# Performance work log

Hardware: AMD Instinct MI355X
Metric: run time of the kernel (lower is better)

Reference implementation:

```python
import jax, jax.numpy as jnp
import numpy as np

N = 100000
E = 1600000
IN_CH = 128
HID = 128
OUT_CH = 1
EPS = 1e-5


def setup_inputs() -> dict:
    key = jax.random.key(0)
    ks = jax.random.split(key, 20)
    x = jax.random.normal(ks[0], (N, IN_CH), dtype=jnp.float32)
    edge_index = jax.random.randint(ks[1], (2, E), 0, N, dtype=jnp.int64)

    def lin(k, fi, fo):
        k1, k2 = jax.random.split(k)
        s = 1.0 / np.sqrt(fi)
        W = jax.random.uniform(k1, (fi, fo), jnp.float32, -s, s)
        b = jax.random.uniform(k2, (fo,), jnp.float32, -s, s)
        return W, b

    W1, b1 = lin(ks[2], IN_CH, HID)
    W2, b2 = lin(ks[3], HID, HID)
    Wf1, bf1 = lin(ks[4], HID, HID)
    Wf2, bf2 = lin(ks[5], HID, HID)
    Wo, bo = lin(ks[6], HID, OUT_CH)

    def bn(k):
        k1, k2, k3, k4 = jax.random.split(k, 4)
        gamma = 1.0 + 0.1 * jax.random.normal(k1, (HID,), jnp.float32)
        beta = 0.1 * jax.random.normal(k2, (HID,), jnp.float32)
        mean = 0.1 * jax.random.normal(k3, (HID,), jnp.float32)
        var = 0.5 + jax.random.uniform(k4, (HID,), jnp.float32)
        return gamma, beta, mean, var

    g1, be1, m1, v1 = bn(ks[7])
    g2, be2, m2, v2 = bn(ks[8])
    g3, be3, m3, v3 = bn(ks[9])

    return dict(x=x, edge_index=edge_index,
                W1=W1, b1=b1, W2=W2, b2=b2,
                Wf1=Wf1, bf1=bf1, Wf2=Wf2, bf2=bf2, Wo=Wo, bo=bo,
                g1=g1, be1=be1, m1=m1, v1=v1,
                g2=g2, be2=be2, m2=m2, v2=v2,
                g3=g3, be3=be3, m3=m3, v3=v3)


def _gcn_conv(x, W, b, src, dst):
    # PyG GCNConv: add self-loops, symmetric normalization deg^-1/2 A deg^-1/2.
    loop = jnp.arange(N, dtype=src.dtype)
    s = jnp.concatenate([src, loop])   # [E+N]
    d = jnp.concatenate([dst, loop])   # [E+N]
    deg = jax.ops.segment_sum(jnp.ones(s.shape[0], x.dtype), d, num_segments=N)
    dinv = jnp.where(deg > 0, jax.lax.rsqrt(deg), 0.0)
    h = x @ W                          # [N, out]
    norm = (dinv[s] * dinv[d])[:, None]  # [E+N, 1]
    msg = h[s] * norm                  # gather + scale, [E+N, out]
    out = jax.ops.segment_sum(msg, d, num_segments=N)  # scatter-add
    return out + b


def _bn(x, gamma, beta, mean, var):
    # BatchNorm1d in inference mode (dropout treated as eval/identity).
    return (x - mean) * jax.lax.rsqrt(var + EPS) * gamma + beta


def reference(x, edge_index, W1, b1, W2, b2, Wf1, bf1, Wf2, bf2, Wo, bo,
              g1, be1, m1, v1, g2, be2, m2, v2, g3, be3, m3, v3):
    src, dst = edge_index[0], edge_index[1]
    h = jax.nn.relu(_bn(_gcn_conv(x, W1, b1, src, dst), g1, be1, m1, v1))
    h = jax.nn.relu(_bn(_gcn_conv(h, W2, b2, src, dst), g2, be2, m2, v2))
    h = jax.nn.relu(_bn(h @ Wf1 + bf1, g3, be3, m3, v3))
    h1 = jax.nn.relu(h @ Wf2 + bf2)
    raw_pred = jax.nn.softplus(h1 @ Wo + bo).reshape(-1)
    return (raw_pred, h1)
```

## Files before the change

### kernel.cpp

```cpp
#include <hip/hip_runtime.h>
#include <math.h>

#define EPS_BN 1e-5f
#define MAXNB 512

typedef __attribute__((ext_vector_type(8))) short bf16x8;
typedef __attribute__((ext_vector_type(4))) float f32x4;
typedef __attribute__((ext_vector_type(2))) float f32x2;

__device__ __forceinline__ ushort f2bf(float f) {
    uint u = __float_as_uint(f);
    u += 0x7FFF + ((u >> 16) & 1);
    return (ushort)(u >> 16);
}
__device__ __forceinline__ float bf2f(uint h) {
    return __uint_as_float(h << 16);
}

__global__ __launch_bounds__(256) void prep_k(const float* __restrict__ W1,
                                              const float* __restrict__ W2,
                                              const float* __restrict__ W3,
                                              const float* __restrict__ W4,
                                              ushort* __restrict__ T1,
                                              ushort* __restrict__ T2,
                                              ushort* __restrict__ T3,
                                              ushort* __restrict__ T4,
                                              int* __restrict__ bcur, int NB, int stride,
                                              const float* __restrict__ b1,
                                              const float* __restrict__ g1,
                                              const float* __restrict__ be1,
                                              const float* __restrict__ m1,
                                              const float* __restrict__ v1,
                                              const float* __restrict__ b2,
                                              const float* __restrict__ g2,
                                              const float* __restrict__ be2,
                                              const float* __restrict__ m2,
                                              const float* __restrict__ v2,
                                              const float* __restrict__ b3,
                                              const float* __restrict__ g3,
                                              const float* __restrict__ be3,
                                              const float* __restrict__ m3,
                                              const float* __restrict__ v3,
                                              float* __restrict__ bnc) {
    if (blockIdx.x == 256) {
        for (int i = threadIdx.x; i < NB; i += 256) bcur[i] = i * stride;
        int cc = threadIdx.x & 127;
        int l2 = threadIdx.x >> 7;
        {
            const float* gg = l2 ? g2 : g1;
            const float* bb = l2 ? be2 : be1;
            const float* mm = l2 ? m2 : m1;
            const float* vv = l2 ? v2 : v1;
            const float* bi = l2 ? b2 : b1;
            float s = gg[cc] * rsqrtf(vv[cc] + EPS_BN);
            float* o = bnc + l2 * 256;
            o[cc] = s;
            o[128 + cc] = bb[cc] + (bi[cc] - mm[cc]) * s;
        }
        if (threadIdx.x < 128) {
            float s = g3[cc] * rsqrtf(v3[cc] + EPS_BN);
            bnc[512 + cc] = s;
            bnc[640 + cc] = be3[cc] + (b3[cc] - m3[cc]) * s;
        }
        return;
    }
    int which = blockIdx.x >> 6;
    const float* W = (which == 0) ? W1 : (which == 1) ? W2 : (which == 2) ? W3 : W4;
    ushort* T = (which == 0) ? T1 : (which == 1) ? T2 : (which == 2) ? T3 : T4;
    int i = (blockIdx.x & 63) * 256 + threadIdx.x;
    int n = i >> 7, k = i & 127;
    int idx = n & 63;
    int nperm = (n & 64) | ((idx & 3) << 4) | (idx >> 2);
    T[nperm * 128 + k] = f2bf(W[k * 128 + n]);
}

__global__ __launch_bounds__(256) void bucketA_k(const int* __restrict__ src,
                                                 const int* __restrict__ dst,
                                                 int* __restrict__ bcur,
                                                 int* __restrict__ coarse, int nE, int NB) {
    __shared__ int cnt[MAXNB];
    __shared__ int basix[MAXNB];
    const int tid = threadIdx.x;
    for (int i = tid; i < NB; i += 256) cnt[i] = 0;
    __syncthreads();
    int base = blockIdx.x * 4096;
    int es[16], ed[16], rk[16];
#pragma unroll
    for (int i = 0; i < 16; i++) {
        int e = base + i * 256 + tid;
        if (e < nE) {
            es[i] = src[e];
            ed[i] = dst[e];
            rk[i] = atomicAdd(&cnt[ed[i] >> 8], 1);
        } else {
            ed[i] = -1;
        }
    }
    __syncthreads();
    for (int i = tid; i < NB; i += 256)
        if (cnt[i]) basix[i] = atomicAdd(&bcur[i], cnt[i]);
    __syncthreads();
#pragma unroll
    for (int i = 0; i < 16; i++) {
        if (ed[i] >= 0)
            coarse[basix[ed[i] >> 8] + rk[i]] = es[i] | ((ed[i] & 255) << 24);
    }
}

__global__ __launch_bounds__(256) void bucketB_k(const int* __restrict__ coarse,
                                                 const int* __restrict__ bcur,
                                                 int2* __restrict__ rowptr,
                                                 int* __restrict__ col,
                                                 float* __restrict__ dinv, int N,
                                                 int stride) {
    __shared__ int cnt[256];
    __shared__ int s[256];
    __shared__ int cur[256];
    const int tid = threadIdx.x;
    const int b = blockIdx.x;
    const int beg = b * stride, end = bcur[b];
    cnt[tid] = 0;
    __syncthreads();
    for (int p = beg + tid; p < end; p += 256)
        atomicAdd(&cnt[((uint)coarse[p]) >> 24], 1);
    __syncthreads();
    int c = cnt[tid];
    s[tid] = c;
    __syncthreads();
    for (int off = 1; off < 256; off <<= 1) {
        int v = (tid >= off) ? s[tid - off] : 0;
        __syncthreads();
        s[tid] += v;
        __syncthreads();
    }
    int ex = s[tid] - c;
    int node = b * 256 + tid;
    if (node < N) {
        rowptr[node] = make_int2(beg + ex, beg + ex + c);
        dinv[node] = rsqrtf((float)c + 1.0f);
    }
    cur[tid] = ex;
    __syncthreads();
    for (int p = beg + tid; p < end; p += 256) {
        int v = coarse[p];
        int r = atomicAdd(&cur[((uint)v) >> 24], 1);
        col[beg + r] = v & 0xFFFFFF;
    }
}

__device__ __forceinline__ void add8p(f32x2* acc, uint2 a) {
    acc[0] += __builtin_amdgcn_cvt_pk_f32_fp8(a.x, false);
    acc[1] += __builtin_amdgcn_cvt_pk_f32_fp8(a.x, true);
    acc[2] += __builtin_amdgcn_cvt_pk_f32_fp8(a.y, false);
    acc[3] += __builtin_amdgcn_cvt_pk_f32_fp8(a.y, true);
}

__global__ __launch_bounds__(256) void gather_k(const unsigned char* __restrict__ h8,
                                                const int2* __restrict__ rowptr,
                                                const int* __restrict__ col,
                                                const float* __restrict__ dinv,
                                                const float* __restrict__ sc,
                                                const float* __restrict__ sh,
                                                ushort* __restrict__ out, int n) {
    int node = blockIdx.x * 4 + (threadIdx.x >> 6);
    if (node >= n) return;
    int lane = threadIdx.x & 63;
    int grp = lane >> 4;
    int li = lane & 15;
    const uint c = (uint)(li * 8);
    const uint c2 = c + (uint)(grp * 2);

    int2 rp = rowptr[node];
    float dd = dinv[node];
    f32x2 s2 = *(const f32x2*)(sc + c2);
    f32x2 h2 = *(const f32x2*)(sh + c2);

    int beg = rp.x, end = rp.y;
    int deg = end - beg;
    int nfull = deg >> 4;

    f32x2 acc[4];
#pragma unroll
    for (int j = 0; j < 4; j++) acc[j] = (f32x2){0.f, 0.f};

    if (grp == 0) {
        uint2 rv = *(const uint2*)(h8 + (((uint)node << 7) | c));
        add8p(acc, rv);
    }

    int pt = beg + grp + (nfull << 4);
    bool v0 = pt < end, v1 = pt + 4 < end, v2 = pt + 8 < end, v3 = pt + 12 < end;
    int t0 = v0 ? __builtin_nontemporal_load(col + pt) : node;
    int t1 = v1 ? __builtin_nontemporal_load(col + pt + 4) : node;
    int t2 = v2 ? __builtin_nontemporal_load(col + pt + 8) : node;
    int t3 = v3 ? __builtin_nontemporal_load(col + pt + 12) : node;

    int p = beg + grp;
    for (int it = 0; it < nfull; ++it, p += 16) {
        int s0 = __builtin_nontemporal_load(col + p);
        int s1 = __builtin_nontemporal_load(col + p + 4);
        int s2i = __builtin_nontemporal_load(col + p + 8);
        int s3 = __builtin_nontemporal_load(col + p + 12);
        uint2 a0 = *(const uint2*)(h8 + (((uint)s0 << 7) | c));
        uint2 a1 = *(const uint2*)(h8 + (((uint)s1 << 7) | c));
        uint2 a2 = *(const uint2*)(h8 + (((uint)s2i << 7) | c));
        uint2 a3 = *(const uint2*)(h8 + (((uint)s3 << 7) | c));
        add8p(acc, a0);
        add8p(acc, a1);
        add8p(acc, a2);
        add8p(acc, a3);
    }
    {
        uint2 a0 = *(const uint2*)(h8 + (((uint)t0 << 7) | c));
        uint2 a1 = *(const uint2*)(h8 + (((uint)t1 << 7) | c));
        uint2 a2 = *(const uint2*)(h8 + (((uint)t2 << 7) | c));
        uint2 a3 = *(const uint2*)(h8 + (((uint)t3 << 7) | c));
        if (!v0) { a0.x = 0u; a0.y = 0u; }
        if (!v1) { a1.x = 0u; a1.y = 0u; }
        if (!v2) { a2.x = 0u; a2.y = 0u; }
        if (!v3) { a3.x = 0u; a3.y = 0u; }
        add8p(acc, a0);
        add8p(acc, a1);
        add8p(acc, a2);
        add8p(acc, a3);
    }
#pragma unroll
    for (int j = 0; j < 4; j++) {
        f32x2 t;
        t.x = __shfl_xor(acc[j].x, 16, 64);
        t.y = __shfl_xor(acc[j].y, 16, 64);
        acc[j] += t;
        t.x = __shfl_xor(acc[j].x, 32, 64);
        t.y = __shfl_xor(acc[j].y, 32, 64);
        acc[j] += t;
    }
    f32x2 pr = (grp == 0) ? acc[0] : (grp == 1) ? acc[1] : (grp == 2) ? acc[2] : acc[3];
    float o0 = fmaxf(fmaf(pr.x * dd, s2.x, h2.x), 0.0f);
    float o1 = fmaxf(fmaf(pr.y * dd, s2.y, h2.y), 0.0f);
    uint r = (uint)f2bf(o0) | ((uint)f2bf(o1) << 16);
    *(uint*)&out[(size_t)node * 128 + c2] = r;
}

template <int MODE, int F32IN>
__global__ __launch_bounds__(256) void mfma_gemm_k(const void* __restrict__ Xin,
                                                   const ushort* __restrict__ Wt,
                                                   const float* __restrict__ dinvp,
                                                   const float* __restrict__ bias,
                                                   const float* __restrict__ scp,
                                                   const float* __restrict__ shp,
                                                   const float* __restrict__ Wo,
                                                   const float* __restrict__ bo,
                                                   float* __restrict__ pred,
                                                   void* __restrict__ Y, int nrows) {
    constexpr int LDK = 136;
    __shared__ ushort sX[64 * LDK];
    __shared__ ushort sW[128 * LDK];
    __shared__ float red[64];
    __shared__ float sD[64];
    const int tid = threadIdx.x;
    const int row0 = blockIdx.x * 64;

#pragma unroll
    for (int i = 0; i < 8; i++) {
        int c = tid + i * 256;
        int r = c >> 4, o = c & 15;
        *(int4*)&sW[r * LDK + o * 8] = *(const int4*)&Wt[r * 128 + o * 8];
    }
    if (F32IN) {
        const float* Xf = (const float*)Xin;
#pragma unroll
        for (int i = 0; i < 8; i++) {
            int c = tid + i * 256;
            int r = c >> 5, o = c & 31;
            int rg = row0 + r;
            if (rg >= nrows) rg = nrows - 1;
            float4 v = *(const float4*)&Xf[(size_t)rg * 128 + o * 4];
            ushort4 u = {f2bf(v.x), f2bf(v.y), f2bf(v.z), f2bf(v.w)};
            *(ushort4*)&sX[r * LDK + o * 4] = u;
        }
    } else {
        const ushort* Xb = (const ushort*)Xin;
#pragma unroll
        for (int i = 0; i < 4; i++) {
            int c = tid + i * 256;
            int r = c >> 4, o = c & 15;
            int rg = row0 + r;
            if (rg >= nrows) rg = nrows - 1;
            *(int4*)&sX[r * LDK + o * 8] = *(const int4*)&Xb[(size_t)rg * 128 + o * 8];
        }
    }
    if (MODE == 2 && tid < 64) red[tid] = 0.0f;
    if (MODE == 0 && tid < 64) {
        int rg = row0 + tid;
        sD[tid] = dinvp[(rg < nrows) ? rg : (nrows - 1)];
    }
    __syncthreads();

    const int wave = tid >> 6, lane = tid & 63;
    const int rw = (wave >> 1) * 32;
    const int cw = (wave & 1) * 64;
    const int lm = lane & 15, lq = lane >> 4;

    f32x4 acc[2][4];
#pragma unroll
    for (int tr = 0; tr < 2; tr++)
#pragma unroll
        for (int tc = 0; tc < 4; tc++) acc[tr][tc] = (f32x4){0.f, 0.f, 0.f, 0.f};

#pragma unroll
    for (int ks = 0; ks < 4; ks++) {
        int kb = ks * 32 + lq * 8;
        bf16x8 a[2], b[4];
#pragma unroll
        for (int tr = 0; tr < 2; tr++)
            a[tr] = *(bf16x8*)&sX[(rw + tr * 16 + lm) * LDK + kb];
#pragma unroll
        for (int tc = 0; tc < 4; tc++)
            b[tc] = *(bf16x8*)&sW[(cw + tc * 16 + lm) * LDK + kb];
#pragma unroll
        for (int tr = 0; tr < 2; tr++)
#pragma unroll
            for (int tc = 0; tc < 4; tc++)
                acc[tr][tc] = __builtin_amdgcn_mfma_f32_16x16x32_bf16(a[tr], b[tc],
                                                                      acc[tr][tc], 0, 0, 0);
    }

    const int c0 = cw + (lm << 2);
    float psc[4], psh[4], woc[4];
#pragma unroll
    for (int tc = 0; tc < 4; tc++) {
        int c = c0 + tc;
        if (MODE == 1) {
            psc[tc] = scp[c];
            psh[tc] = shp[c];
        } else if (MODE == 2) {
            psh[tc] = bias[c];
            woc[tc] = Wo[c];
        }
    }
    float part[8];
    if (MODE == 2) {
#pragma unroll
        for (int i = 0; i < 8; i++) part[i] = 0.0f;
    }
#pragma unroll
    for (int tr = 0; tr < 2; tr++) {
#pragma unroll
        for (int r = 0; r < 4; r++) {
            int lrow = rw + tr * 16 + lq * 4 + r;
            int row = row0 + lrow;
            if (row >= nrows) continue;
            if (MODE == 0) {
                float dd = sD[lrow];
                uint q = __builtin_amdgcn_cvt_pk_fp8_f32(acc[tr][0][r] * dd,
                                                         acc[tr][1][r] * dd, 0u, false);
                q = __builtin_amdgcn_cvt_pk_fp8_f32(acc[tr][2][r] * dd,
                                                    acc[tr][3][r] * dd, q, true);
                *(uint*)((unsigned char*)Y + (size_t)row * 128 + c0) = q;
            } else if (MODE == 1) {
                float o0 = fmaxf(fmaf(acc[tr][0][r], psc[0], psh[0]), 0.0f);
                float o1 = fmaxf(fmaf(acc[tr][1][r], psc[1], psh[1]), 0.0f);
                float o2 = fmaxf(fmaf(acc[tr][2][r], psc[2], psh[2]), 0.0f);
                float o3 = fmaxf(fmaf(acc[tr][3][r], psc[3], psh[3]), 0.0f);
                uint2 st;
                st.x = (uint)f2bf(o0) | ((uint)f2bf(o1) << 16);
                st.y = (uint)f2bf(o2) | ((uint)f2bf(o3) << 16);
                *(uint2*)((ushort*)Y + (size_t)row * 128 + c0) = st;
            } else {
                float o0 = fmaxf(acc[tr][0][r] + psh[0], 0.0f);
                float o1 = fmaxf(acc[tr][1][r] + psh[1], 0.0f);
                float o2 = fmaxf(acc[tr][2][r] + psh[2], 0.0f);
                float o3 = fmaxf(acc[tr][3][r] + psh[3], 0.0f);
                float4 st = {o0, o1, o2, o3};
                *(float4*)((float*)Y + (size_t)row * 128 + c0) = st;
                part[tr * 4 + r] = fmaf(o0, woc[0],
                                   fmaf(o1, woc[1],
                                   fmaf(o2, woc[2],
                                   fmaf(o3, woc[3], part[tr * 4 + r]))));
            }
        }
    }
    if (MODE == 2) {
#pragma unroll
        for (int tr = 0; tr < 2; tr++)
#pragma unroll
            for (int r = 0; r < 4; r++)
                atomicAdd(&red[rw + tr * 16 + lq * 4 + r], part[tr * 4 + r]);
        __syncthreads();
        if (tid < 64) {
            int row = row0 + tid;
            if (row < nrows) {
                float xv = red[tid] + bo[0];
                pred[row] = fmaxf(xv, 0.0f) + log1pf(expf(-fabsf(xv)));
            }
        }
    }
}

extern "C" void kernel_launch(void* const* d_in, const int* in_sizes, int n_in,
                              void* d_out, int out_size, void* d_ws, size_t ws_size,
                              hipStream_t stream) {
    const float* x = (const float*)d_in[0];
    const int* ei = (const int*)d_in[1];
    const int N = in_sizes[0] / 128;
    const int E = in_sizes[1] / 2;
    const int* srcv = ei;
    const int* dstv = ei + E;
    const float* W1 = (const float*)d_in[2];  const float* b1 = (const float*)d_in[3];
    const float* W2 = (const float*)d_in[4];  const float* b2 = (const float*)d_in[5];
    const float* Wf1 = (const float*)d_in[6]; const float* bf1 = (const float*)d_in[7];
    const float* Wf2 = (const float*)d_in[8]; const float* bf2 = (const float*)d_in[9];
    const float* Wo = (const float*)d_in[10]; const float* bo = (const float*)d_in[11];
    const float* g1 = (const float*)d_in[12], *be1 = (const float*)d_in[13],
               *m1 = (const float*)d_in[14], *v1 = (const float*)d_in[15];
    const float* g2 = (const float*)d_in[16], *be2 = (const float*)d_in[17],
               *m2 = (const float*)d_in[18], *v2 = (const float*)d_in[19];
    const float* g3 = (const float*)d_in[20], *be3 = (const float*)d_in[21],
               *m3 = (const float*)d_in[22], *v3 = (const float*)d_in[23];

    char* ws = (char*)d_ws;
    size_t off = 0;
    auto carve = [&](size_t bytes) {
        char* p = ws + off;
        off = (off + bytes + 255) & ~(size_t)255;
        return p;
    };
    const int NB = (N + 255) >> 8;
    const int STRIDE = ((E / NB + 511) + 255) & ~255;
    int* bcur = (int*)carve((size_t)MAXNB * 4);
    int2* rowptr = (int2*)carve((size_t)N * 8);
    int* col = (int*)carve((size_t)NB * STRIDE * 4);
    int* coarse = (int*)carve((size_t)NB * STRIDE * 4);
    float* dinv = (float*)carve((size_t)N * 4);
    unsigned char* bufA8 = (unsigned char*)carve((size_t)N * 128);
    ushort* bufB = (ushort*)carve((size_t)N * 128 * 2);
    ushort* bufC = (ushort*)carve((size_t)N * 128 * 2);
    ushort* Wt1 = (ushort*)carve(128 * 128 * 2);
    ushort* Wt2 = (ushort*)carve(128 * 128 * 2);
    ushort* Wtf1 = (ushort*)carve(128 * 128 * 2);
    ushort* Wtf2 = (ushort*)carve(128 * 128 * 2);
    float* bnc = (float*)carve(768 * 4);

    float* out_pred = (float*)d_out;
    float* out_h1 = out_pred + N;

    const int gblocks = (N + 63) / 64;
    const int tblocks = (E + 4095) / 4096;
    const int wblocks = (N + 3) / 4;

    prep_k<<<257, 256, 0, stream>>>(W1, W2, Wf1, Wf2, Wt1, Wt2, Wtf1, Wtf2, bcur, NB,
                                    STRIDE, b1, g1, be1, m1, v1, b2, g2, be2, m2, v2,
                                    bf1, g3, be3, m3, v3, bnc);
    bucketA_k<<<tblocks, 256, 0, stream>>>(srcv, dstv, bcur, coarse, E, NB);
    bucketB_k<<<NB, 256, 0, stream>>>(coarse, bcur, rowptr, col, dinv, N, STRIDE);

    mfma_gemm_k<0, 1><<<gblocks, 256, 0, stream>>>(x, Wt1, dinv, nullptr, nullptr,
                                                   nullptr, nullptr, nullptr, nullptr,
                                                   bufA8, N);
    gather_k<<<wblocks, 256, 0, stream>>>(bufA8, rowptr, col, dinv,
                                          bnc, bnc + 128, bufB, N);
    mfma_gemm_k<0, 0><<<gblocks, 256, 0, stream>>>(bufB, Wt2, dinv, nullptr, nullptr,
                                                   nullptr, nullptr, nullptr, nullptr,
                                                   bufA8, N);
    gather_k<<<wblocks, 256, 0, stream>>>(bufA8, rowptr, col, dinv,
                                          bnc + 256, bnc + 384, bufB, N);
    mfma_gemm_k<1, 0><<<gblocks, 256, 0, stream>>>(bufB, Wtf1, nullptr, nullptr,
                                                   bnc + 512, bnc + 640, nullptr,
                                                   nullptr, nullptr, bufC, N);
    mfma_gemm_k<2, 0><<<gblocks, 256, 0, stream>>>(bufC, Wtf2, nullptr, bf2, nullptr,
                                                   nullptr, Wo, bo,
                                                   out_pred, out_h1, N);
}
```

Before: 337.4 us.

## Load GEMM MFMA operands directly from global memory, dropping LDS staging

The dense GEMM kernel no longer stages the X tile and the weight matrix in shared memory. Each lane now reads its MFMA A and B fragments straight from global memory, converting fp32 input to bf16 in registers, and dinv is read per row instead of from LDS. This removes the LDS fill, the barrier and the LDS reads, and cuts LDS use so more blocks can be resident. In exchange, weight and X fragments are re-read from global/L2 by several waves with less coalesced access patterns.

```diff
diff --git a/kernel.cpp b/kernel.cpp
--- a/kernel.cpp
+++ b/kernel.cpp
@@ -12,9 +12,6 @@
     uint u = __float_as_uint(f);
     u += 0x7FFF + ((u >> 16) & 1);
     return (ushort)(u >> 16);
-}
-__device__ __forceinline__ float bf2f(uint h) {
-    return __uint_as_float(h << 16);
 }
 
 __global__ __launch_bounds__(256) void prep_k(const float* __restrict__ W1,
@@ -241,6 +238,15 @@
     *(uint*)&out[(size_t)node * 128 + c2] = r;
 }
 
+__device__ __forceinline__ bf16x8 ldrow_f32(const float* p) {
+    float4 v0 = *(const float4*)p;
+    float4 v1 = *(const float4*)(p + 4);
+    union { bf16x8 v; ushort u[8]; } r;
+    r.u[0] = f2bf(v0.x); r.u[1] = f2bf(v0.y); r.u[2] = f2bf(v0.z); r.u[3] = f2bf(v0.w);
+    r.u[4] = f2bf(v1.x); r.u[5] = f2bf(v1.y); r.u[6] = f2bf(v1.z); r.u[7] = f2bf(v1.w);
+    return r.v;
+}
+
 template <int MODE, int F32IN>
 __global__ __launch_bounds__(256) void mfma_gemm_k(const void* __restrict__ Xin,
                                                    const ushort* __restrict__ Wt,
@@ -252,55 +258,24 @@
                                                    const float* __restrict__ bo,
                                                    float* __restrict__ pred,
                                                    void* __restrict__ Y, int nrows) {
-    constexpr int LDK = 136;
-    __shared__ ushort sX[64 * LDK];
-    __shared__ ushort sW[128 * LDK];
     __shared__ float red[64];
-    __shared__ float sD[64];
     const int tid = threadIdx.x;
     const int row0 = blockIdx.x * 64;
-
-#pragma unroll
-    for (int i = 0; i < 8; i++) {
-        int c = tid + i * 256;
-        int r = c >> 4, o = c & 15;
-        *(int4*)&sW[r * LDK + o * 8] = *(const int4*)&Wt[r * 128 + o * 8];
-    }
-    if (F32IN) {
-        const float* Xf = (const float*)Xin;
-#pragma unroll
-        for (int i = 0; i < 8; i++) {
-            int c = tid + i * 256;
-            int r = c >> 5, o = c & 31;
-            int rg = row0 + r;
-            if (rg >= nrows) rg = nrows - 1;
-            float4 v = *(const float4*)&Xf[(size_t)rg * 128 + o * 4];
-            ushort4 u = {f2bf(v.x), f2bf(v.y), f2bf(v.z), f2bf(v.w)};
-            *(ushort4*)&sX[r * LDK + o * 4] = u;
-        }
-    } else {
-        const ushort* Xb = (const ushort*)Xin;
-#pragma unroll
-        for (int i = 0; i < 4; i++) {
-            int c = tid + i * 256;
-            int r = c >> 4, o = c & 15;
-            int rg = row0 + r;
-            if (rg >= nrows) rg = nrows - 1;
-            *(int4*)&sX[r * LDK + o * 8] = *(const int4*)&Xb[(size_t)rg * 128 + o * 8];
-        }
-    }
-    if (MODE == 2 && tid < 64) red[tid] = 0.0f;
-    if (MODE == 0 && tid < 64) {
-        int rg = row0 + tid;
-        sD[tid] = dinvp[(rg < nrows) ? rg : (nrows - 1)];
-    }
-    __syncthreads();
-
     const int wave = tid >> 6, lane = tid & 63;
     const int rw = (wave >> 1) * 32;
     const int cw = (wave & 1) * 64;
     const int lm = lane & 15, lq = lane >> 4;
 
+    if (MODE == 2) {
+        if (tid < 64) red[tid] = 0.0f;
+        __syncthreads();
+    }
+
+    int ra0 = row0 + rw + lm;
+    int ra1 = ra0 + 16;
+    if (ra0 >= nrows) ra0 = nrows - 1;
+    if (ra1 >= nrows) ra1 = nrows - 1;
+
     f32x4 acc[2][4];
 #pragma unroll
     for (int tr = 0; tr < 2; tr++)
@@ -311,12 +286,18 @@
     for (int ks = 0; ks < 4; ks++) {
         int kb = ks * 32 + lq * 8;
         bf16x8 a[2], b[4];
-#pragma unroll
-        for (int tr = 0; tr < 2; tr++)
-            a[tr] = *(bf16x8*)&sX[(rw + tr * 16 + lm) * LDK + kb];
+        if (F32IN) {
+            const float* Xf = (const float*)Xin;
+            a[0] = ldrow_f32(&Xf[(size_t)ra0 * 128 + kb]);
+            a[1] = ldrow_f32(&Xf[(size_t)ra1 * 128 + kb]);
+        } else {
+            const ushort* Xb = (const ushort*)Xin;
+            a[0] = *(const bf16x8*)&Xb[(size_t)ra0 * 128 + kb];
+            a[1] = *(const bf16x8*)&Xb[(size_t)ra1 * 128 + kb];
+        }
 #pragma unroll
         for (int tc = 0; tc < 4; tc++)
-            b[tc] = *(bf16x8*)&sW[(cw + tc * 16 + lm) * LDK + kb];
+            b[tc] = *(const bf16x8*)&Wt[(cw + tc * 16 + lm) * 128 + kb];
 #pragma unroll
         for (int tr = 0; tr < 2; tr++)
 #pragma unroll
@@ -347,11 +328,10 @@
     for (int tr = 0; tr < 2; tr++) {
 #pragma unroll
         for (int r = 0; r < 4; r++) {
-            int lrow = rw + tr * 16 + lq * 4 + r;
-            int row = row0 + lrow;
+            int row = row0 + rw + tr * 16 + lq * 4 + r;
             if (row >= nrows) continue;
             if (MODE == 0) {
-                float dd = sD[lrow];
+                float dd = dinvp[row];
                 uint q = __builtin_amdgcn_cvt_pk_fp8_f32(acc[tr][0][r] * dd,
                                                          acc[tr][1][r] * dd, 0u, false);
                 q = __builtin_amdgcn_cvt_pk_fp8_f32(acc[tr][2][r] * dd,
@@ -384,8 +364,10 @@
 #pragma unroll
         for (int tr = 0; tr < 2; tr++)
 #pragma unroll
-            for (int r = 0; r < 4; r++)
-                atomicAdd(&red[rw + tr * 16 + lq * 4 + r], part[tr * 4 + r]);
+            for (int r = 0; r < 4; r++) {
+                int lrow = rw + tr * 16 + lq * 4 + r;
+                atomicAdd(&red[lrow], part[tr * 4 + r]);
+            }
         __syncthreads();
         if (tid < 64) {
             int row = row0 + tid;
```

New measurement: 390.4 us. 1.16x slower.

## Load GEMM tiles via global_load_lds with XOR-swizzled LDS and pre-swizzled global layouts

Applied to the files above, without the earlier changes.

Replaces register-staged global-to-LDS copies in the MFMA GEMM with direct global_load_lds 16-byte transfers, dropping the padded LDS stride in favour of an XOR swizzle for bank conflicts. To make direct copies land in swizzled order, the bf16 weight transposes and the bf16 intermediate activation buffers are written pre-swizzled by prep_k, the aggregation kernel and the GEMM epilogue. The dinv preload to shared memory is replaced by a direct global read per row. This couples data layout across several kernels, and any consumer that reads these buffers unswizzled would break. Buffers gain padding to absorb clamped or overrun loads.

```diff
diff --git a/kernel.cpp b/kernel.cpp
--- a/kernel.cpp
+++ b/kernel.cpp
@@ -13,9 +13,12 @@
     u += 0x7FFF + ((u >> 16) & 1);
     return (ushort)(u >> 16);
 }
-__device__ __forceinline__ float bf2f(uint h) {
-    return __uint_as_float(h << 16);
-}
+
+__device__ __forceinline__ void gload_lds16(const void* g, void* l) {
+    __builtin_amdgcn_global_load_lds((const unsigned int*)g, (unsigned int*)l, 16, 0, 0);
+}
+
+#define SWZ(row, byte_in_row) ((byte_in_row) ^ (((row) & 7) << 4))
 
 __global__ __launch_bounds__(256) void prep_k(const float* __restrict__ W1,
                                               const float* __restrict__ W2,
@@ -71,7 +74,8 @@
     int n = i >> 7, k = i & 127;
     int idx = n & 63;
     int nperm = (n & 64) | ((idx & 3) << 4) | (idx >> 2);
-    T[nperm * 128 + k] = f2bf(W[k * 128 + n]);
+    uint boff = ((uint)nperm << 8) + SWZ(nperm, (uint)k * 2);
+    *(ushort*)((char*)T + boff) = f2bf(W[k * 128 + n]);
 }
 
 __global__ __launch_bounds__(256) void bucketA_k(const int* __restrict__ src,
@@ -238,7 +242,8 @@
     float o0 = fmaxf(fmaf(pr.x * dd, s2.x, h2.x), 0.0f);
     float o1 = fmaxf(fmaf(pr.y * dd, s2.y, h2.y), 0.0f);
     uint r = (uint)f2bf(o0) | ((uint)f2bf(o1) << 16);
-    *(uint*)&out[(size_t)node * 128 + c2] = r;
+    uint boff = ((uint)node << 8) + SWZ((uint)node, c2 * 2);
+    *(uint*)((char*)out + boff) = r;
 }
 
 template <int MODE, int F32IN>
@@ -252,51 +257,47 @@
                                                    const float* __restrict__ bo,
                                                    float* __restrict__ pred,
                                                    void* __restrict__ Y, int nrows) {
-    constexpr int LDK = 136;
-    __shared__ ushort sX[64 * LDK];
-    __shared__ ushort sW[128 * LDK];
+    __shared__ ushort sX[64 * 128];
+    __shared__ ushort sW[128 * 128];
     __shared__ float red[64];
-    __shared__ float sD[64];
     const int tid = threadIdx.x;
     const int row0 = blockIdx.x * 64;
-
-#pragma unroll
-    for (int i = 0; i < 8; i++) {
-        int c = tid + i * 256;
-        int r = c >> 4, o = c & 15;
-        *(int4*)&sW[r * LDK + o * 8] = *(const int4*)&Wt[r * 128 + o * 8];
+    const int wave = tid >> 6, lane = tid & 63;
+
+    {
+        const char* gW = (const char*)Wt;
+#pragma unroll
+        for (int i = 0; i < 8; i++) {
+            int base = (wave * 8 + i) * 1024;
+            gload_lds16(gW + base + lane * 16, (char*)sW + base);
+        }
     }
     if (F32IN) {
         const float* Xf = (const float*)Xin;
 #pragma unroll
         for (int i = 0; i < 8; i++) {
-            int c = tid + i * 256;
-            int r = c >> 5, o = c & 31;
+            int cidx = tid + i * 256;
+            int r = cidx >> 5, o = cidx & 31;
             int rg = row0 + r;
             if (rg >= nrows) rg = nrows - 1;
             float4 v = *(const float4*)&Xf[(size_t)rg * 128 + o * 4];
             ushort4 u = {f2bf(v.x), f2bf(v.y), f2bf(v.z), f2bf(v.w)};
-            *(ushort4*)&sX[r * LDK + o * 4] = u;
+            *(ushort4*)((char*)sX + (r << 8) + SWZ(r, o * 8)) = u;
         }
     } else {
-        const ushort* Xb = (const ushort*)Xin;
+        const char* gX = (const char*)Xin;
 #pragma unroll
         for (int i = 0; i < 4; i++) {
-            int c = tid + i * 256;
-            int r = c >> 4, o = c & 15;
-            int rg = row0 + r;
+            int base = (wave * 4 + i) * 1024;
+            int off = base + lane * 16;
+            int rg = row0 + (off >> 8);
             if (rg >= nrows) rg = nrows - 1;
-            *(int4*)&sX[r * LDK + o * 8] = *(const int4*)&Xb[(size_t)rg * 128 + o * 8];
+            gload_lds16(gX + (size_t)rg * 256 + (off & 255), (char*)sX + base);
         }
     }
     if (MODE == 2 && tid < 64) red[tid] = 0.0f;
-    if (MODE == 0 && tid < 64) {
-        int rg = row0 + tid;
-        sD[tid] = dinvp[(rg < nrows) ? rg : (nrows - 1)];
-    }
-    __syncthreads();
-
-    const int wave = tid >> 6, lane = tid & 63;
+    __syncthreads();
+
     const int rw = (wave >> 1) * 32;
     const int cw = (wave & 1) * 64;
     const int lm = lane & 15, lq = lane >> 4;
@@ -309,14 +310,18 @@
 
 #pragma unroll
     for (int ks = 0; ks < 4; ks++) {
-        int kb = ks * 32 + lq * 8;
+        int kbyte = ks * 64 + lq * 16;
         bf16x8 a[2], b[4];
 #pragma unroll
-        for (int tr = 0; tr < 2; tr++)
-            a[tr] = *(bf16x8*)&sX[(rw + tr * 16 + lm) * LDK + kb];
-#pragma unroll
-        for (int tc = 0; tc < 4; tc++)
-            b[tc] = *(bf16x8*)&sW[(cw + tc * 16 + lm) * LDK + kb];
+        for (int tr = 0; tr < 2; tr++) {
+            int r = rw + tr * 16 + lm;
+            a[tr] = *(bf16x8*)((char*)sX + (r << 8) + SWZ(r, kbyte));
+        }
+#pragma unroll
+        for (int tc = 0; tc < 4; tc++) {
+            int r = cw + tc * 16 + lm;
+            b[tc] = *(bf16x8*)((char*)sW + (r << 8) + SWZ(r, kbyte));
+        }
 #pragma unroll
         for (int tr = 0; tr < 2; tr++)
 #pragma unroll
@@ -347,11 +352,10 @@
     for (int tr = 0; tr < 2; tr++) {
 #pragma unroll
         for (int r = 0; r < 4; r++) {
-            int lrow = rw + tr * 16 + lq * 4 + r;
-            int row = row0 + lrow;
+            int row = row0 + rw + tr * 16 + lq * 4 + r;
             if (row >= nrows) continue;
             if (MODE == 0) {
-                float dd = sD[lrow];
+                float dd = dinvp[row];
                 uint q = __builtin_amdgcn_cvt_pk_fp8_f32(acc[tr][0][r] * dd,
                                                          acc[tr][1][r] * dd, 0u, false);
                 q = __builtin_amdgcn_cvt_pk_fp8_f32(acc[tr][2][r] * dd,
@@ -365,7 +369,8 @@
                 uint2 st;
                 st.x = (uint)f2bf(o0) | ((uint)f2bf(o1) << 16);
                 st.y = (uint)f2bf(o2) | ((uint)f2bf(o3) << 16);
-                *(uint2*)((ushort*)Y + (size_t)row * 128 + c0) = st;
+                uint boff = ((uint)row << 8) + SWZ((uint)row, (uint)(c0 * 2));
+                *(uint2*)((char*)Y + boff) = st;
             } else {
                 float o0 = fmaxf(acc[tr][0][r] + psh[0], 0.0f);
                 float o1 = fmaxf(acc[tr][1][r] + psh[1], 0.0f);
@@ -384,8 +389,10 @@
 #pragma unroll
         for (int tr = 0; tr < 2; tr++)
 #pragma unroll
-            for (int r = 0; r < 4; r++)
-                atomicAdd(&red[rw + tr * 16 + lq * 4 + r], part[tr * 4 + r]);
+            for (int r = 0; r < 4; r++) {
+                int lrow = rw + tr * 16 + lq * 4 + r;
+                atomicAdd(&red[lrow], part[tr * 4 + r]);
+            }
         __syncthreads();
         if (tid < 64) {
             int row = row0 + tid;
@@ -432,9 +439,9 @@
     int* col = (int*)carve((size_t)NB * STRIDE * 4);
     int* coarse = (int*)carve((size_t)NB * STRIDE * 4);
     float* dinv = (float*)carve((size_t)N * 4);
-    unsigned char* bufA8 = (unsigned char*)carve((size_t)N * 128);
-    ushort* bufB = (ushort*)carve((size_t)N * 128 * 2);
-    ushort* bufC = (ushort*)carve((size_t)N * 128 * 2);
+    unsigned char* bufA8 = (unsigned char*)carve((size_t)N * 128 + 16384);
+    ushort* bufB = (ushort*)carve((size_t)N * 128 * 2 + 16384);
+    ushort* bufC = (ushort*)carve((size_t)N * 128 * 2 + 16384);
     ushort* Wt1 = (ushort*)carve(128 * 128 * 2);
     ushort* Wt2 = (ushort*)carve(128 * 128 * 2);
     ushort* Wtf1 = (ushort*)carve(128 * 128 * 2);
```

New measurement: 334.4 us. About the same (-0.9%).
